# Optimization experiments

Measured on AMD Instinct MI355X. Metric: run time of the kernel, lower is better.

The kernel has to match this reference:

```python
import jax, jax.numpy as jnp
import numpy as np

H = W = 56
WS = 7        # window size
SS = 3        # shift size
NH = 8        # num heads
EPS = 1e-5


def _rel_pos_index(ws):
    coords = np.stack(np.meshgrid(np.arange(ws), np.arange(ws), indexing='ij')).reshape(2, -1)
    rel = (coords[:, :, None] - coords[:, None, :]).transpose(1, 2, 0)  # (N,N,2)
    rel[:, :, 0] += ws - 1
    rel[:, :, 1] += ws - 1
    rel[:, :, 0] *= 2 * ws - 1
    return rel.sum(-1)  # (N,N) int


def _attn_mask(h, w, ws, ss):
    img = np.zeros((h, w))
    sl = (slice(0, -ws), slice(-ws, -ss), slice(-ss, None))
    cnt = 0
    for hs in sl:
        for wsl in sl:
            img[hs, wsl] = cnt
            cnt += 1
    mw = img.reshape(h // ws, ws, w // ws, ws).transpose(0, 2, 1, 3).reshape(-1, ws * ws)  # (nW,N)
    diff = mw[:, None, :] - mw[:, :, None]  # (nW,N,N)
    return np.where(diff != 0, -100.0, 0.0).astype(np.float32)


def _ln(x, w, b):
    m = x.mean(-1, keepdims=True)
    v = ((x - m) ** 2).mean(-1, keepdims=True)
    return (x - m) * jax.lax.rsqrt(v + EPS) * w + b


def setup_inputs() -> dict:
    key = jax.random.key(0)
    ks = jax.random.split(key, 8)
    C = 256
    s = 0.02
    return {
        'x': jax.random.normal(ks[0], (32, H * W, C), jnp.float32),
        'norm1_w': jnp.ones((C,), jnp.float32),
        'norm1_b': jnp.zeros((C,), jnp.float32),
        'qkv_w': jax.random.normal(ks[1], (3 * C, C), jnp.float32) * s,
        'qkv_b': jnp.zeros((3 * C,), jnp.float32),
        'proj_w': jax.random.normal(ks[2], (C, C), jnp.float32) * s,
        'proj_b': jnp.zeros((C,), jnp.float32),
        'rel_bias_table': jax.random.normal(ks[3], (169, NH), jnp.float32) * s,
        'norm2_w': jnp.ones((C,), jnp.float32),
        'norm2_b': jnp.zeros((C,), jnp.float32),
        'fc1_w': jax.random.normal(ks[4], (4 * C, C), jnp.float32) * s,
        'fc1_b': jnp.zeros((4 * C,), jnp.float32),
        'fc2_w': jax.random.normal(ks[5], (C, 4 * C), jnp.float32) * s,
        'fc2_b': jnp.zeros((C,), jnp.float32),
    }


def reference(x, norm1_w, norm1_b, qkv_w, qkv_b, proj_w, proj_b, rel_bias_table,
              norm2_w, norm2_b, fc1_w, fc1_b, fc2_w, fc2_b):
    B, L, C = x.shape
    N = WS * WS
    nW = (H // WS) * (W // WS)
    hd = C // NH
    scale = hd ** (-0.5)

    rel_idx = jnp.asarray(_rel_pos_index(WS))          # (N,N)
    mask = jnp.asarray(_attn_mask(H, W, WS, SS))       # (nW,N,N)

    shortcut = x
    h = _ln(x, norm1_w, norm1_b).reshape(B, H, W, C)
    h = jnp.roll(h, (-SS, -SS), axis=(1, 2))
    # window partition -> (B*nW, N, C)
    hw = h.reshape(B, H // WS, WS, W // WS, WS, C).transpose(0, 1, 3, 2, 4, 5).reshape(-1, N, C)

    qkv = hw @ qkv_w.T + qkv_b                          # (B_, N, 3C)
    qkv = qkv.reshape(-1, N, 3, NH, hd).transpose(2, 0, 3, 1, 4)
    q, k, v = qkv[0] * scale, qkv[1], qkv[2]            # (B_, NH, N, hd)

    attn = jnp.einsum('bhnd,bhmd->bhnm', q, k)          # (B_, NH, N, N)
    bias = rel_bias_table[rel_idx.reshape(-1)].reshape(N, N, NH).transpose(2, 0, 1)
    attn = attn + bias[None]
    attn = attn.reshape(B, nW, NH, N, N) + mask[None, :, None]
    attn = jax.nn.softmax(attn.reshape(-1, NH, N, N), axis=-1)

    out = jnp.einsum('bhnm,bhmd->bhnd', attn, v)        # (B_, NH, N, hd)
    out = out.transpose(0, 2, 1, 3).reshape(-1, N, C)
    out = out @ proj_w.T + proj_b

    # window reverse + unshift
    out = out.reshape(B, H // WS, W // WS, WS, WS, C).transpose(0, 1, 3, 2, 4, 5).reshape(B, H, W, C)
    out = jnp.roll(out, (SS, SS), axis=(1, 2)).reshape(B, L, C)

    x = shortcut + out
    y = _ln(x, norm2_w, norm2_b)
    y = jax.nn.gelu(y @ fc1_w.T + fc1_b, approximate=False) @ fc2_w.T + fc2_b
    return x + y
```

## Files before the change

kernel.cpp:

```cpp
#include <hip/hip_runtime.h>
#include <hip/hip_bf16.h>
#include <cstddef>

using bf16 = __hip_bfloat16;
typedef __bf16 bf16x8 __attribute__((ext_vector_type(8)));
typedef float f32x4 __attribute__((ext_vector_type(4)));

typedef __attribute__((address_space(1))) const void* gas1_t;
typedef __attribute__((address_space(3))) void* las3_t;

__device__ __forceinline__ void g2lds16(const void* g, void* l) {
  __builtin_amdgcn_global_load_lds((gas1_t)g, (las3_t)l, 16, 0, 0);
}

#define M_ROWS 100352
#define CDIM   256

__global__ void cvt_bf16(const float* __restrict__ in, bf16* __restrict__ out, int n) {
  int i = blockIdx.x * 256 + threadIdx.x;
  if (i < n) out[i] = __float2bfloat16(in[i]);
}

__global__ __launch_bounds__(256) void ln1_shift_kernel(
    const float* __restrict__ x, const float* __restrict__ w, const float* __restrict__ bb,
    bf16* __restrict__ hw) {
  int row = blockIdx.x * 4 + (threadIdx.x >> 6);
  int l = threadIdx.x & 63;
  int b_ = row / 49;
  int n  = row - b_ * 49;
  int bidx = b_ >> 6;
  int wi = b_ & 63;
  int wh = wi >> 3, ww = wi & 7;
  int r = n / 7, c = n - r * 7;
  int y = wh * 7 + r + 3;  if (y >= 56) y -= 56;
  int xx = ww * 7 + c + 3; if (xx >= 56) xx -= 56;
  size_t src = ((size_t)bidx * 3136 + (size_t)(y * 56 + xx)) * 256 + l * 4;
  float4 v = *reinterpret_cast<const float4*>(x + src);
  float s  = v.x + v.y + v.z + v.w;
  float ss = v.x * v.x + v.y * v.y + v.z * v.z + v.w * v.w;
#pragma unroll
  for (int off = 32; off > 0; off >>= 1) {
    s  += __shfl_xor(s, off);
    ss += __shfl_xor(ss, off);
  }
  float mean = s * (1.f / 256.f);
  float var  = ss * (1.f / 256.f) - mean * mean;
  float rs   = rsqrtf(var + 1e-5f);
  int ch = l * 4;
  float4 wv = *reinterpret_cast<const float4*>(w + ch);
  float4 bv = *reinterpret_cast<const float4*>(bb + ch);
  bf16 o[4];
  o[0] = __float2bfloat16((v.x - mean) * rs * wv.x + bv.x);
  o[1] = __float2bfloat16((v.y - mean) * rs * wv.y + bv.y);
  o[2] = __float2bfloat16((v.z - mean) * rs * wv.z + bv.z);
  o[3] = __float2bfloat16((v.w - mean) * rs * wv.w + bv.w);
  *reinterpret_cast<short4*>(hw + (size_t)row * 256 + ch) = *reinterpret_cast<const short4*>(o);
}

__global__ __launch_bounds__(256) void ln_kernel(
    const float* __restrict__ xin, const float* __restrict__ w, const float* __restrict__ bb,
    bf16* __restrict__ out) {
  int row = blockIdx.x * 4 + (threadIdx.x >> 6);
  int l = threadIdx.x & 63;
  size_t src = (size_t)row * 256 + l * 4;
  float4 v = *reinterpret_cast<const float4*>(xin + src);
  float s  = v.x + v.y + v.z + v.w;
  float ss = v.x * v.x + v.y * v.y + v.z * v.z + v.w * v.w;
#pragma unroll
  for (int off = 32; off > 0; off >>= 1) {
    s  += __shfl_xor(s, off);
    ss += __shfl_xor(ss, off);
  }
  float mean = s * (1.f / 256.f);
  float var  = ss * (1.f / 256.f) - mean * mean;
  float rs   = rsqrtf(var + 1e-5f);
  int ch = l * 4;
  float4 wv = *reinterpret_cast<const float4*>(w + ch);
  float4 bv = *reinterpret_cast<const float4*>(bb + ch);
  bf16 o[4];
  o[0] = __float2bfloat16((v.x - mean) * rs * wv.x + bv.x);
  o[1] = __float2bfloat16((v.y - mean) * rs * wv.y + bv.y);
  o[2] = __float2bfloat16((v.z - mean) * rs * wv.z + bv.z);
  o[3] = __float2bfloat16((v.w - mean) * rs * wv.w + bv.w);
  *reinterpret_cast<short4*>(out + src) = *reinterpret_cast<const short4*>(o);
}

__global__ __launch_bounds__(256) void attn_mfma_kernel(
    const bf16* __restrict__ qkv, const float* __restrict__ bias_table,
    bf16* __restrict__ attn_out) {
  __shared__ char smem[4 * 12992];
  const int tid = threadIdx.x;
  const int wid = tid >> 6;
  const int lane = tid & 63;
  const int lrow = lane & 15;
  const int kseg = lane >> 4;
  const int b_ = blockIdx.x >> 1;
  const int h = ((blockIdx.x & 1) << 2) + wid;
  const int wi = b_ & 63;
  const int wh = wi >> 3, ww = wi & 7;

  char* L = smem + wid * 12992;

  const bf16* src0 = qkv + (size_t)b_ * (49 * 768) + h * 32;
#pragma unroll
  for (int t = 0; t < 3; ++t) {
    const bf16* src = src0 + t * 256;
    char* dst = L + t * 4096;
#pragma unroll
    for (int it = 0; it < 4; ++it) {
      int c = it * 64 + lane;
      if (c < 196)
        g2lds16(src + (size_t)(c >> 2) * 768 + (c & 3) * 8, dst + c * 16);
    }
  }
  if (lane < 60) {
    int4 z = {0, 0, 0, 0};
    *reinterpret_cast<int4*>(L + 8192 + (196 + lane) * 16) = z;
  }
  float* blds = reinterpret_cast<float*>(L + 12288);
  for (int e = lane; e < 169; e += 64) blds[e] = bias_table[e * 8 + h];

  asm volatile("s_waitcnt vmcnt(0) lgkmcnt(0)" ::: "memory");

  bf16x8 qf[4], kf[4];
#pragma unroll
  for (int im = 0; im < 4; ++im)
    qf[im] = *reinterpret_cast<const bf16x8*>(L + (16 * im + lrow) * 64 + kseg * 16);
#pragma unroll
  for (int jn = 0; jn < 4; ++jn)
    kf[jn] = *reinterpret_cast<const bf16x8*>(L + 4096 + (16 * jn + lrow) * 64 + kseg * 16);
  f32x4 S[4][4] = {};
#pragma unroll
  for (int im = 0; im < 4; ++im)
#pragma unroll
    for (int jn = 0; jn < 4; ++jn)
      S[im][jn] = __builtin_amdgcn_mfma_f32_16x16x32_bf16(qf[im], kf[jn], S[im][jn], 0, 0, 0);

  const float scale = 0.17677669529663689f;
  int fj[4], rj[4], cj[4];
  bool jbad[4];
#pragma unroll
  for (int jn = 0; jn < 4; ++jn) {
    int j = 16 * jn + lrow;
    int rr = (j * 37) >> 8;
    int cc = j - rr * 7;
    rj[jn] = rr; cj[jn] = cc;
    int yj = wh * 7 + rr, xj = ww * 7 + cc;
    fj[jn] = (yj < 49 ? 0 : (yj < 53 ? 1 : 2)) * 3 + (xj < 49 ? 0 : (xj < 53 ? 1 : 2));
    jbad[jn] = (j >= 49);
  }
#pragma unroll
  for (int im = 0; im < 4; ++im) {
#pragma unroll
    for (int r = 0; r < 4; ++r) {
      int i = 16 * im + 4 * kseg + r;
      int ri = (i * 37) >> 8;
      int ci = i - ri * 7;
      int yi = wh * 7 + ri, xi = ww * 7 + ci;
      int fi = (yi < 49 ? 0 : (yi < 53 ? 1 : 2)) * 3 + (xi < 49 ? 0 : (xi < 53 ? 1 : 2));
#pragma unroll
      for (int jn = 0; jn < 4; ++jn) {
        float s = S[im][jn][r] * scale + blds[(ri - rj[jn] + 6) * 13 + (ci - cj[jn] + 6)];
        S[im][jn][r] = (fi != fj[jn] || jbad[jn]) ? -1e30f : s;
      }
    }
  }

#pragma unroll
  for (int im = 0; im < 4; ++im) {
#pragma unroll
    for (int r = 0; r < 4; ++r) {
      float m = fmaxf(fmaxf(S[im][0][r], S[im][1][r]), fmaxf(S[im][2][r], S[im][3][r]));
      m = fmaxf(m, __shfl_xor(m, 1));
      m = fmaxf(m, __shfl_xor(m, 2));
      m = fmaxf(m, __shfl_xor(m, 4));
      m = fmaxf(m, __shfl_xor(m, 8));
      float e0 = __expf(S[im][0][r] - m);
      float e1 = __expf(S[im][1][r] - m);
      float e2 = __expf(S[im][2][r] - m);
      float e3 = __expf(S[im][3][r] - m);
      float sum = e0 + e1 + e2 + e3;
      sum += __shfl_xor(sum, 1);
      sum += __shfl_xor(sum, 2);
      sum += __shfl_xor(sum, 4);
      sum += __shfl_xor(sum, 8);
      float inv = 1.f / sum;
      int i = 16 * im + 4 * kseg + r;
      int xorv = (i & 7) << 4;
      float ev[4] = {e0, e1, e2, e3};
#pragma unroll
      for (int jn = 0; jn < 4; ++jn) {
        bf16 pb = __float2bfloat16(ev[jn] * inv);
        *reinterpret_cast<unsigned short*>(L + i * 128 + (((16 * jn + lrow) * 2) ^ xorv)) =
            *reinterpret_cast<unsigned short*>(&pb);
      }
    }
  }

  f32x4 O[4][2] = {};
#pragma unroll
  for (int ks = 0; ks < 2; ++ks) {
    bf16x8 pa[4];
#pragma unroll
    for (int im = 0; im < 4; ++im) {
      int row = 16 * im + lrow;
      int byte = (ks * 64 + kseg * 16) ^ ((row & 7) << 4);
      pa[im] = *reinterpret_cast<const bf16x8*>(L + row * 128 + byte);
    }
#pragma unroll
    for (int dn = 0; dn < 2; ++dn) {
      bf16x8 vf;
#pragma unroll
      for (int jj = 0; jj < 8; ++jj) {
        int j = ks * 32 + kseg * 8 + jj;
        reinterpret_cast<unsigned short*>(&vf)[jj] =
            *reinterpret_cast<const unsigned short*>(L + 8192 + j * 64 + (16 * dn + lrow) * 2);
      }
#pragma unroll
      for (int im = 0; im < 4; ++im)
        O[im][dn] = __builtin_amdgcn_mfma_f32_16x16x32_bf16(pa[im], vf, O[im][dn], 0, 0, 0);
    }
  }

  bf16* outb = attn_out + (size_t)b_ * 49 * 256 + h * 32;
#pragma unroll
  for (int im = 0; im < 4; ++im) {
#pragma unroll
    for (int r = 0; r < 4; ++r) {
      int i = 16 * im + 4 * kseg + r;
      if (i < 49) {
#pragma unroll
        for (int dn = 0; dn < 2; ++dn)
          outb[(size_t)i * 256 + 16 * dn + lrow] = __float2bfloat16(O[im][dn][r]);
      }
    }
  }
}

enum { EPI_BF16 = 0, EPI_GELU = 1, EPI_PROJ = 2, EPI_ADD = 3 };

template <int EPI>
__global__ __launch_bounds__(256) void gemm_kernel(
    const bf16* __restrict__ A, const bf16* __restrict__ Bw,
    const float* __restrict__ bias, int N, int K,
    void* __restrict__ outp, const float* __restrict__ addf) {
  __shared__ __align__(16) bf16 As[128][32];
  __shared__ __align__(16) bf16 Bs[128][32];
  __shared__ int tdst[128];

  const int tid = threadIdx.x;
  const int m0 = blockIdx.x * 128;
  const int n0 = blockIdx.y * 128;

  if constexpr (EPI == EPI_PROJ) {
    if (tid < 128) {
      int m = m0 + tid;
      int b_ = m / 49;
      int n = m - b_ * 49;
      int bidx = b_ >> 6;
      int wi = b_ & 63;
      int wh = wi >> 3, ww = wi & 7;
      int r = n / 7, c = n - r * 7;
      int y = wh * 7 + r + 3;  if (y >= 56) y -= 56;
      int xx = ww * 7 + c + 3; if (xx >= 56) xx -= 56;
      tdst[tid] = bidx * 3136 + y * 56 + xx;
    }
  }

  const int wv = tid >> 6;
  const int wm = wv >> 1, wn = wv & 1;
  const int l = tid & 63;
  const int lrow = l & 15;
  const int kseg = l >> 4;

  f32x4 acc[4][4] = {};

  for (int k0 = 0; k0 < K; k0 += 32) {
#pragma unroll
    for (int i = 0; i < 2; ++i) {
      int idx = i * 256 + tid;
      const bf16* ga = A + (size_t)(m0 + (idx >> 2)) * K + (k0 + (idx & 3) * 8);
      g2lds16(ga, (char*)(&As[0][0]) + idx * 16);
      const bf16* gb = Bw + (size_t)(n0 + (idx >> 2)) * K + (k0 + (idx & 3) * 8);
      g2lds16(gb, (char*)(&Bs[0][0]) + idx * 16);
    }
    __syncthreads();

    bf16x8 af[4], bfr[4];
#pragma unroll
    for (int im = 0; im < 4; ++im)
      af[im] = *reinterpret_cast<const bf16x8*>(&As[wm * 64 + im * 16 + lrow][kseg * 8]);
#pragma unroll
    for (int in_ = 0; in_ < 4; ++in_)
      bfr[in_] = *reinterpret_cast<const bf16x8*>(&Bs[wn * 64 + in_ * 16 + lrow][kseg * 8]);
#pragma unroll
    for (int im = 0; im < 4; ++im)
#pragma unroll
      for (int in_ = 0; in_ < 4; ++in_)
        acc[im][in_] = __builtin_amdgcn_mfma_f32_16x16x32_bf16(af[im], bfr[in_], acc[im][in_], 0, 0, 0);
    __syncthreads();
  }

  const int col = l & 15;
#pragma unroll
  for (int im = 0; im < 4; ++im) {
#pragma unroll
    for (int in_ = 0; in_ < 4; ++in_) {
      int nch = n0 + wn * 64 + in_ * 16 + col;
      float bv = bias[nch];
#pragma unroll
      for (int r = 0; r < 4; ++r) {
        int m = m0 + wm * 64 + im * 16 + (l >> 4) * 4 + r;
        float val = acc[im][in_][r] + bv;
        if constexpr (EPI == EPI_BF16) {
          ((bf16*)outp)[(size_t)m * N + nch] = __float2bfloat16(val);
        } else if constexpr (EPI == EPI_GELU) {
          val = 0.5f * val * (1.f + erff(val * 0.70710678118654752f));
          ((bf16*)outp)[(size_t)m * N + nch] = __float2bfloat16(val);
        } else if constexpr (EPI == EPI_PROJ) {
          int td = tdst[m - m0];
          size_t o = (size_t)td * 256 + nch;
          ((float*)outp)[o] = addf[o] + val;
        } else {
          size_t o = (size_t)m * N + nch;
          ((float*)outp)[o] = addf[o] + val;
        }
      }
    }
  }
}

extern "C" void kernel_launch(void* const* d_in, const int* in_sizes, int n_in,
                              void* d_out, int out_size, void* d_ws, size_t ws_size,
                              hipStream_t stream) {
  const float* x      = (const float*)d_in[0];
  const float* n1w    = (const float*)d_in[1];
  const float* n1b    = (const float*)d_in[2];
  const float* qkv_w  = (const float*)d_in[3];
  const float* qkv_b  = (const float*)d_in[4];
  const float* proj_w = (const float*)d_in[5];
  const float* proj_b = (const float*)d_in[6];
  const float* relb   = (const float*)d_in[7];
  const float* n2w    = (const float*)d_in[8];
  const float* n2b    = (const float*)d_in[9];
  const float* fc1_w  = (const float*)d_in[10];
  const float* fc1_b  = (const float*)d_in[11];
  const float* fc2_w  = (const float*)d_in[12];
  const float* fc2_b  = (const float*)d_in[13];
  float* out = (float*)d_out;
  char* ws = (char*)d_ws;

  const size_t HW_BYTES   = (size_t)M_ROWS * 256 * 2;
  const size_t QKV_BYTES  = (size_t)M_ROWS * 768 * 2;
  const size_t YIN_BYTES  = (size_t)M_ROWS * 256 * 2;

  char* regA = ws;
  bf16* hw    = (bf16*)regA;
  bf16* qkvb  = (bf16*)(regA + HW_BYTES);
  bf16* h1    = (bf16*)regA;
  char* p = regA + HW_BYTES + QKV_BYTES;
  bf16* y_in   = (bf16*)p;             p += YIN_BYTES;
  bf16* wq  = (bf16*)p;                p += (size_t)768 * 256 * 2;
  bf16* wp  = (bf16*)p;                p += (size_t)256 * 256 * 2;
  bf16* wf1 = (bf16*)p;                p += (size_t)1024 * 256 * 2;
  bf16* wf2 = (bf16*)p;                p += (size_t)256 * 1024 * 2;
  float* x_new = out;
  (void)ws_size; (void)in_sizes; (void)n_in; (void)out_size;

  cvt_bf16<<<768, 256, 0, stream>>>(qkv_w, wq, 768 * 256);
  cvt_bf16<<<256, 256, 0, stream>>>(proj_w, wp, 256 * 256);
  cvt_bf16<<<1024, 256, 0, stream>>>(fc1_w, wf1, 1024 * 256);
  cvt_bf16<<<1024, 256, 0, stream>>>(fc2_w, wf2, 256 * 1024);

  ln1_shift_kernel<<<M_ROWS / 4, 256, 0, stream>>>(x, n1w, n1b, hw);

  gemm_kernel<EPI_BF16><<<dim3(784, 6), 256, 0, stream>>>(hw, wq, qkv_b, 768, 256, qkvb, nullptr);

  attn_mfma_kernel<<<4096, 256, 0, stream>>>(qkvb, relb, hw);

  gemm_kernel<EPI_PROJ><<<dim3(784, 2), 256, 0, stream>>>(hw, wp, proj_b, 256, 256, x_new, x);

  ln_kernel<<<M_ROWS / 4, 256, 0, stream>>>(x_new, n2w, n2b, y_in);

  gemm_kernel<EPI_GELU><<<dim3(784, 8), 256, 0, stream>>>(y_in, wf1, fc1_b, 1024, 256, h1, nullptr);

  gemm_kernel<EPI_ADD><<<dim3(784, 2), 256, 0, stream>>>(h1, wf2, fc2_b, 256, 1024, out, x_new);
}
```

Measured before the change: 593.4 us.

## Double-buffer GEMM LDS tiles and remap block ids across XCDs

The GEMM kernel now keeps two LDS buffers per operand. It issues the global-to-LDS loads for the next K tile before running the MFMAs on the current one, so memory latency can overlap with compute. The 2D grid becomes a 1D grid, and block ids are permuted so that consecutive tile indices land on the same XCD (round-robin of 8), which should improve L2 reuse of the shared A rows. This doubles LDS use per block and may lower occupancy. With only one sync per iteration, it also relies on the async LDS loads being complete at the barrier.

```diff
diff --git a/kernel.cpp b/kernel.cpp
--- a/kernel.cpp
+++ b/kernel.cpp
@@ -242,15 +242,20 @@
 template <int EPI>
 __global__ __launch_bounds__(256) void gemm_kernel(
     const bf16* __restrict__ A, const bf16* __restrict__ Bw,
-    const float* __restrict__ bias, int N, int K,
+    const float* __restrict__ bias, int NY, int N, int K,
     void* __restrict__ outp, const float* __restrict__ addf) {
-  __shared__ __align__(16) bf16 As[128][32];
-  __shared__ __align__(16) bf16 Bs[128][32];
+  __shared__ __align__(16) bf16 As[2][128][32];
+  __shared__ __align__(16) bf16 Bs[2][128][32];
   __shared__ int tdst[128];
 
   const int tid = threadIdx.x;
-  const int m0 = blockIdx.x * 128;
-  const int n0 = blockIdx.y * 128;
+  const int bid = blockIdx.x;
+  const int nblk = gridDim.x;
+  const int w = (bid & 7) * (nblk >> 3) + (bid >> 3);
+  const int bx = w / NY;
+  const int by = w - bx * NY;
+  const int m0 = bx * 128;
+  const int n0 = by * 128;
 
   if constexpr (EPI == EPI_PROJ) {
     if (tid < 128) {
@@ -275,30 +280,46 @@
 
   f32x4 acc[4][4] = {};
 
-  for (int k0 = 0; k0 < K; k0 += 32) {
+  const int nk = K >> 5;
+
+  auto stage = [&](int buf, int kt) {
+    int k0 = kt << 5;
 #pragma unroll
     for (int i = 0; i < 2; ++i) {
       int idx = i * 256 + tid;
-      const bf16* ga = A + (size_t)(m0 + (idx >> 2)) * K + (k0 + (idx & 3) * 8);
-      g2lds16(ga, (char*)(&As[0][0]) + idx * 16);
-      const bf16* gb = Bw + (size_t)(n0 + (idx >> 2)) * K + (k0 + (idx & 3) * 8);
-      g2lds16(gb, (char*)(&Bs[0][0]) + idx * 16);
-    }
-    __syncthreads();
+      g2lds16(A + (size_t)(m0 + (idx >> 2)) * K + (k0 + (idx & 3) * 8),
+              (char*)(&As[buf][0][0]) + idx * 16);
+    }
+#pragma unroll
+    for (int i = 0; i < 2; ++i) {
+      int idx = i * 256 + tid;
+      g2lds16(Bw + (size_t)(n0 + (idx >> 2)) * K + (k0 + (idx & 3) * 8),
+              (char*)(&Bs[buf][0][0]) + idx * 16);
+    }
+  };
+
+  stage(0, 0);
+  __syncthreads();
+
+  int cur = 0;
+  for (int kt = 0; kt < nk; ++kt) {
+    if (kt + 1 < nk) stage(cur ^ 1, kt + 1);
 
     bf16x8 af[4], bfr[4];
 #pragma unroll
     for (int im = 0; im < 4; ++im)
-      af[im] = *reinterpret_cast<const bf16x8*>(&As[wm * 64 + im * 16 + lrow][kseg * 8]);
+      af[im] = *reinterpret_cast<const bf16x8*>(&As[cur][wm * 64 + im * 16 + lrow][kseg * 8]);
 #pragma unroll
     for (int in_ = 0; in_ < 4; ++in_)
-      bfr[in_] = *reinterpret_cast<const bf16x8*>(&Bs[wn * 64 + in_ * 16 + lrow][kseg * 8]);
+      bfr[in_] = *reinterpret_cast<const bf16x8*>(&Bs[cur][wn * 64 + in_ * 16 + lrow][kseg * 8]);
 #pragma unroll
     for (int im = 0; im < 4; ++im)
 #pragma unroll
       for (int in_ = 0; in_ < 4; ++in_)
         acc[im][in_] = __builtin_amdgcn_mfma_f32_16x16x32_bf16(af[im], bfr[in_], acc[im][in_], 0, 0, 0);
+
     __syncthreads();
+    cur ^= 1;
   }
 
   const int col = l & 15;
@@ -374,15 +395,15 @@
 
   ln1_shift_kernel<<<M_ROWS / 4, 256, 0, stream>>>(x, n1w, n1b, hw);
 
-  gemm_kernel<EPI_BF16><<<dim3(784, 6), 256, 0, stream>>>(hw, wq, qkv_b, 768, 256, qkvb, nullptr);
+  gemm_kernel<EPI_BF16><<<784 * 6, 256, 0, stream>>>(hw, wq, qkv_b, 6, 768, 256, qkvb, nullptr);
 
   attn_mfma_kernel<<<4096, 256, 0, stream>>>(qkvb, relb, hw);
 
-  gemm_kernel<EPI_PROJ><<<dim3(784, 2), 256, 0, stream>>>(hw, wp, proj_b, 256, 256, x_new, x);
+  gemm_kernel<EPI_PROJ><<<784 * 2, 256, 0, stream>>>(hw, wp, proj_b, 2, 256, 256, x_new, x);
 
   ln_kernel<<<M_ROWS / 4, 256, 0, stream>>>(x_new, n2w, n2b, y_in);
 
-  gemm_kernel<EPI_GELU><<<dim3(784, 8), 256, 0, stream>>>(y_in, wf1, fc1_b, 1024, 256, h1, nullptr);
-
-  gemm_kernel<EPI_ADD><<<dim3(784, 2), 256, 0, stream>>>(h1, wf2, fc2_b, 256, 1024, out, x_new);
-}
+  gemm_kernel<EPI_GELU><<<784 * 8, 256, 0, stream>>>(y_in, wf1, fc1_b, 8, 1024, 256, h1, nullptr);
+
+  gemm_kernel<EPI_ADD><<<784 * 2, 256, 0, stream>>>(h1, wf2, fc2_b, 2, 256, 1024, out, x_new);
+}
```

Result: faster. 548.4 us (-7.6%).
